# Kernel optimization log

Hardware: AMD Instinct MI355X
Metric: run time of the kernel (lower is better)

The kernel has to match this reference:

```python
import jax, jax.numpy as jnp
import numpy as np
from functools import partial

BETA = 0.9
THR = 1.0
NUM_STEPS = 50
SLOPE = 15.0
BN_EPS = 1e-5
NHID = 250
NCLS = 10

@jax.custom_vjp
def spike_fn(x):
    return (x > 0).astype(x.dtype)

def _spike_fwd(x):
    return spike_fn(x), x

def _spike_bwd(x, g):
    # snntorch fast_sigmoid surrogate: grad = 1 / (slope*|x| + 1)^2
    return (g / (SLOPE * jnp.abs(x) + 1.0) ** 2,)

spike_fn.defvjp(_spike_fwd, _spike_bwd)

def conv1d(x, w, b, stride=1):
    # x: [B,C,L], w: [O,I,K]
    y = jax.lax.conv_general_dilated(x, w, (stride,), 'VALID',
                                     dimension_numbers=('NCH', 'OIH', 'NCH'))
    return y + b[None, :, None]

def bn_eval(x, g, b, m, v):
    inv = g / jnp.sqrt(v + BN_EPS)
    return (x - m[None, :, None]) * inv[None, :, None] + b[None, :, None]

def lif_step(mem, cur):
    # snntorch Leaky (reset_mechanism='subtract'): reset uses detached spike of previous mem
    reset = jax.lax.stop_gradient((mem > THR).astype(mem.dtype))
    mem = BETA * mem + cur - reset * THR
    spk = spike_fn(mem - THR)
    return mem, spk

def maxpool4(x):
    # MaxPool1d(4) on [B,C,L]
    return jax.lax.reduce_window(x, -jnp.inf, jax.lax.max, (1, 1, 4), (1, 1, 4), 'VALID')

def get_embedding(x, c1w, c1b, bn1g, bn1b, bn1m, bn1v, c2w, c2b, bn2g, bn2b, bn2m, bn2v,
                  fc1w, fc1b, fcsw, fcsb):
    B = x.shape[0]
    # input-invariant part of the per-step loop (conv1+BN1 on x)
    cur1 = bn_eval(conv1d(x, c1w, c1b, stride=4), bn1g, bn1b, bn1m, bn1v)  # [B,16,1981]

    def step(carry, _):
        mem1, mem2, mem3 = carry
        mem1, spk1 = lif_step(mem1, cur1)
        pooled = maxpool4(spk1)                                   # [B,16,495]
        cur2 = bn_eval(conv1d(pooled, c2w, c2b), bn2g, bn2b, bn2m, bn2v)  # [B,32,493]
        mem2, spk2 = lif_step(mem2, cur2)
        flat = spk2.reshape(B, -1)                                # [B,15776]
        cur3 = flat @ fc1w.T + fc1b                               # dropout is eval -> identity
        mem3, spk3 = lif_step(mem3, cur3)
        return (mem1, mem2, mem3), spk3

    carry0 = (jnp.zeros_like(cur1),
              jnp.zeros((B, 32, 493), cur1.dtype),
              jnp.zeros((B, NHID), cur1.dtype))
    _, spk_rec = jax.lax.scan(step, carry0, None, length=NUM_STEPS)  # [T,B,250]

    firing_rate = spk_rec.sum(axis=0)                                 # [B,250]
    latency = jnp.argmax(spk_rec, axis=0).astype(x.dtype) / NUM_STEPS # first-spike idx
    comb = jnp.concatenate([firing_rate, latency], axis=1)            # [B,500]
    out = comb @ fcsw.T + fcsb                                        # [B,128]
    norm = jnp.maximum(jnp.linalg.norm(out, axis=1, keepdims=True), 1e-12)
    return out / norm

def setup_inputs() -> dict:
    key = jax.random.key(0)
    ks = jax.random.split(key, 16)
    B, L = 32, 8000
    d = {}
    d['x1'] = jax.random.normal(ks[0], (B, 1, L), jnp.float32)
    d['x2'] = jax.random.normal(ks[1], (B, 1, L), jnp.float32)
    d['c1w'] = jax.random.normal(ks[2], (16, 1, 80), jnp.float32) * 0.1
    d['c1b'] = jax.random.normal(ks[3], (16,), jnp.float32) * 0.1
    d['bn1g'] = jnp.ones((16,), jnp.float32)
    d['bn1b'] = jnp.zeros((16,), jnp.float32)
    d['bn1m'] = jax.random.normal(ks[4], (16,), jnp.float32) * 0.1
    d['bn1v'] = jax.random.uniform(ks[5], (16,), jnp.float32, 0.5, 1.5)
    d['c2w'] = jax.random.normal(ks[6], (32, 16, 3), jnp.float32) * 0.1
    d['c2b'] = jax.random.normal(ks[7], (32,), jnp.float32) * 0.1
    d['bn2g'] = jnp.ones((32,), jnp.float32)
    d['bn2b'] = jnp.zeros((32,), jnp.float32)
    d['bn2m'] = jax.random.normal(ks[8], (32,), jnp.float32) * 0.1
    d['bn2v'] = jax.random.uniform(ks[9], (32,), jnp.float32, 0.5, 1.5)
    d['fc1w'] = jax.random.normal(ks[10], (NHID, 15776), jnp.float32) * 0.02
    d['fc1b'] = jax.random.normal(ks[11], (NHID,), jnp.float32) * 0.02
    d['fcsw'] = jax.random.normal(ks[12], (128, 2 * NHID), jnp.float32) * 0.05
    d['fcsb'] = jax.random.normal(ks[13], (128,), jnp.float32) * 0.05
    return d

def reference(x1, x2, c1w, c1b, bn1g, bn1b, bn1m, bn1v, c2w, c2b, bn2g, bn2b, bn2m, bn2v,
              fc1w, fc1b, fcsw, fcsb):
    params = (c1w, c1b, bn1g, bn1b, bn1m, bn1v, c2w, c2b, bn2g, bn2b, bn2m, bn2v,
              fc1w, fc1b, fcsw, fcsb)
    emb1 = get_embedding(x1, *params)
    emb2 = get_embedding(x2, *params)
    return (emb1, emb2)
```

## Files before the change

kernel.cpp:

```cpp
#include <hip/hip_runtime.h>
#include <math.h>
#include <stdint.h>

#define BETA 0.9f
#define THR 1.0f
#define T_STEPS 50
#define BN_EPS 1e-5f

#define NITEM 64
#define C1 16
#define L1 1981
#define L1P 1984
#define P4 495
#define C2 32
#define L2 493
#define L2PAD 496
#define KTOT 15872
#define KREAL 15776
#define NFC 250
#define NPAD 256
#define KSPLIT 16
#define KRANGE 992
#define KSTEPS 31
#define NKTILE 496
#define MROWS 3200
#define TSLICE 1015808

#define OFF_CUR1 0UL
#define OFF_POOL 8126464UL
#define OFF_SPK2 34340864UL
#define OFF_WT   85131264UL
#define OFF_PART 101384192UL
#define OFF_COMB 127598592UL
#define OFF_CUR3 16384UL

typedef __attribute__((ext_vector_type(8))) short bf16x8;
typedef __attribute__((ext_vector_type(4))) float f32x4;

__device__ __forceinline__ uint32_t f32_to_bf16_rne(float f) {
  uint32_t u = __float_as_uint(f);
  return (u + 0x7FFFu + ((u >> 16) & 1u)) >> 16;
}

__device__ __forceinline__ bf16x8 frag_from_bytes(uint2 a) {
  union { uint32_t u[4]; bf16x8 v; } c;
  c.u[0] = (a.x & 0x00010001u) * 0x3F80u;
  c.u[1] = ((a.x >> 8) & 0x00010001u) * 0x3F80u;
  c.u[2] = (a.y & 0x00010001u) * 0x3F80u;
  c.u[3] = ((a.y >> 8) & 0x00010001u) * 0x3F80u;
  return c.v;
}

__global__ __launch_bounds__(256) void k_wt(const float* __restrict__ fc1w,
                                            uint8_t* __restrict__ wTf) {
  int kt = blockIdx.x;
  int n = threadIdx.x;
  int wv = n >> 6, ni = (n >> 4) & 3, r16 = n & 15;
  uint32_t h16[32], l16[32];
#pragma unroll
  for (int kl = 0; kl < 32; ++kl) {
    int k = kt * 32 + kl;
    int oc = k / L2PAD;
    int pos = k - oc * L2PAD;
    float w = 0.f;
    if (pos < L2 && n < NFC) w = fc1w[n * KREAL + oc * L2 + pos];
    uint32_t hb = f32_to_bf16_rne(w);
    float hf = __uint_as_float(hb << 16);
    h16[kl] = hb;
    l16[kl] = f32_to_bf16_rne(w - hf);
  }
  uint8_t* tb = wTf + (size_t)kt * 32768 + wv * 8192 + ni * 2048;
#pragma unroll
  for (int g = 0; g < 4; ++g) {
    int b = g * 8;
    uint4 h;
    h.x = h16[b + 0] | (h16[b + 2] << 16);
    h.y = h16[b + 1] | (h16[b + 3] << 16);
    h.z = h16[b + 4] | (h16[b + 6] << 16);
    h.w = h16[b + 5] | (h16[b + 7] << 16);
    *reinterpret_cast<uint4*>(tb + (g * 16 + r16) * 16) = h;
    uint4 l;
    l.x = l16[b + 0] | (l16[b + 2] << 16);
    l.y = l16[b + 1] | (l16[b + 3] << 16);
    l.z = l16[b + 4] | (l16[b + 6] << 16);
    l.w = l16[b + 5] | (l16[b + 7] << 16);
    *reinterpret_cast<uint4*>(tb + 1024 + (g * 16 + r16) * 16) = l;
  }
}

__global__ __launch_bounds__(256) void k_conv1(const float* __restrict__ x1, const float* __restrict__ x2,
                                               const float* __restrict__ c1w, const float* __restrict__ c1b,
                                               const float* __restrict__ g, const float* __restrict__ bb,
                                               const float* __restrict__ mn, const float* __restrict__ vr,
                                               float* __restrict__ cur1) {
  __shared__ __align__(16) float xs[1104];
  int item = blockIdx.y;
  int pc = blockIdx.x;
  int tid = threadIdx.x;
  const float* x = (item < 32 ? x1 : x2) + (item & 31) * 8000;
  int xoff = pc * 1024;
  for (int i = tid; i < 1100; i += 256) {
    int gi = xoff + i;
    xs[i] = (gi < 8000) ? x[gi] : 0.f;
  }
  __syncthreads();
  int p = pc * 256 + tid;
  bool pv = (p < L1);
  const float4* xs4 = reinterpret_cast<const float4*>(xs);
  for (int c = 0; c < C1; ++c) {
    float s = g[c] / sqrtf(vr[c] + BN_EPS);
    float sh = (c1b[c] - mn[c]) * s + bb[c];
    const float4* w4 = reinterpret_cast<const float4*>(c1w + c * 80);
    float acc = 0.f;
#pragma unroll
    for (int k4 = 0; k4 < 20; ++k4) {
      float4 wv4 = w4[k4];
      float4 xv = xs4[tid + k4];
      acc += wv4.x * xv.x; acc += wv4.y * xv.y;
      acc += wv4.z * xv.z; acc += wv4.w * xv.w;
    }
    if (pv) cur1[(item * C1 + c) * L1P + p] = acc * s + sh;
  }
}

__global__ __launch_bounds__(256) void k_lif1(const float* __restrict__ cur1,
                                              uint8_t* __restrict__ pooledT) {
  int item = blockIdx.y;
  int g = threadIdx.x & 3;
  int p4 = blockIdx.x * 64 + (threadIdx.x >> 2);
  if (p4 >= P4) return;
  float4 cv[4];
#pragma unroll
  for (int j = 0; j < 4; ++j)
    cv[j] = *reinterpret_cast<const float4*>(cur1 + ((size_t)item * C1 + g * 4 + j) * L1P + 4 * p4);
  float m[4][4];
#pragma unroll
  for (int j = 0; j < 4; ++j)
#pragma unroll
    for (int r = 0; r < 4; ++r) m[j][r] = 0.f;
  uint32_t* out = reinterpret_cast<uint32_t*>(pooledT + ((size_t)item * 50 * 512 + p4) * 16 + g * 4);
  for (int t = 0; t < T_STEPS; ++t) {
    uint32_t pk = 0;
#pragma unroll
    for (int j = 0; j < 4; ++j) {
      int s = 0;
#pragma unroll
      for (int r = 0; r < 4; ++r) {
        float rst = (m[j][r] > THR) ? 1.f : 0.f;
        float cvv = (r == 0) ? cv[j].x : (r == 1) ? cv[j].y : (r == 2) ? cv[j].z : cv[j].w;
        m[j][r] = BETA * m[j][r] + cvv - rst;
        s |= (m[j][r] > THR);
      }
      pk |= ((uint32_t)s) << (8 * j);
    }
    out[t * 2048] = pk;
  }
}

__global__ __launch_bounds__(256) void k_conv2(const uint8_t* __restrict__ pooledT,
                                               const float* __restrict__ c2w, const float* __restrict__ c2b,
                                               const float* __restrict__ g, const float* __restrict__ bb,
                                               const float* __restrict__ mn, const float* __restrict__ vr,
                                               uint32_t* __restrict__ spk2) {
  int item = blockIdx.y;
  int pt = blockIdx.x;
  int tid = threadIdx.x;
  int lane = tid & 63, wv = tid >> 6;
  int r16 = lane & 15, kg = lane >> 4;
  bf16x8 bw[2][2][2];
  float sh[2];
#pragma unroll
  for (int nt = 0; nt < 2; ++nt) {
    int oc = nt * 16 + r16;
    float s2 = g[oc] * rsqrtf(vr[oc] + BN_EPS);
    sh[nt] = (c2b[oc] - mn[oc]) * s2 + bb[oc];
#pragma unroll
    for (int kt = 0; kt < 2; ++kt) {
      uint32_t h[8], l[8];
#pragma unroll
      for (int j = 0; j < 8; ++j) {
        int k = kt * 32 + kg * 8 + j;
        int tap = k >> 4, ic = k & 15;
        float raw = (tap < 3) ? c2w[oc * 48 + ic * 3 + tap] * s2 : 0.f;
        uint32_t hb = f32_to_bf16_rne(raw);
        float hf = __uint_as_float(hb << 16);
        h[j] = hb;
        l[j] = f32_to_bf16_rne(raw - hf);
      }
      union { uint32_t u[4]; bf16x8 v; } ch_, cl_;
      ch_.u[0] = h[0] | (h[2] << 16); ch_.u[1] = h[1] | (h[3] << 16);
      ch_.u[2] = h[4] | (h[6] << 16); ch_.u[3] = h[5] | (h[7] << 16);
      cl_.u[0] = l[0] | (l[2] << 16); cl_.u[1] = l[1] | (l[3] << 16);
      cl_.u[2] = l[4] | (l[6] << 16); cl_.u[3] = l[5] | (l[7] << 16);
      bw[nt][kt][0] = ch_.v;
      bw[nt][kt][1] = cl_.v;
    }
  }
  const uint8_t* base = pooledT + (size_t)item * 50 * 8192;
  int rowA = pt * 64 + wv * 16 + r16;
  size_t off0 = (size_t)(rowA + (kg >> 1)) * 16 + 8 * (kg & 1);
  size_t off1 = (size_t)(rowA + 2) * 16 + 8 * (kg & 1);
  uint2 na0 = *reinterpret_cast<const uint2*>(base + off0);
  uint2 na1 = *reinterpret_cast<const uint2*>(base + off1);
  float mem[2][4] = {{0.f, 0.f, 0.f, 0.f}, {0.f, 0.f, 0.f, 0.f}};
  int pos_base = pt * 64 + wv * 16 + kg * 4;
  bool dostore = pos_base < L2PAD;
  int k0a = r16 * L2PAD + pos_base;
  int k0b = (16 + r16) * L2PAD + pos_base;
  uint32_t sidx0 = (uint32_t)(k0a >> 5) * 512u + (uint32_t)item * 8u + ((uint32_t)(k0a >> 2) & 7u);
  uint32_t sidx1 = (uint32_t)(k0b >> 5) * 512u + (uint32_t)item * 8u + ((uint32_t)(k0b >> 2) & 7u);
  for (int t = 0; t < T_STEPS; ++t) {
    uint2 a0 = na0, a1 = na1;
    const uint8_t* nb = base + (size_t)((t + 1 < T_STEPS) ? t + 1 : t) * 8192;
    na0 = *reinterpret_cast<const uint2*>(nb + off0);
    na1 = *reinterpret_cast<const uint2*>(nb + off1);
    bf16x8 af0 = frag_from_bytes(a0);
    bf16x8 af1 = frag_from_bytes(a1);
    uint32_t st[2];
#pragma unroll
    for (int nt = 0; nt < 2; ++nt) {
      f32x4 acc = (f32x4){0.f, 0.f, 0.f, 0.f};
      acc = __builtin_amdgcn_mfma_f32_16x16x32_bf16(af0, bw[nt][0][0], acc, 0, 0, 0);
      acc = __builtin_amdgcn_mfma_f32_16x16x32_bf16(af1, bw[nt][1][0], acc, 0, 0, 0);
      acc = __builtin_amdgcn_mfma_f32_16x16x32_bf16(af0, bw[nt][0][1], acc, 0, 0, 0);
      acc = __builtin_amdgcn_mfma_f32_16x16x32_bf16(af1, bw[nt][1][1], acc, 0, 0, 0);
      uint32_t packed = 0;
#pragma unroll
      for (int r = 0; r < 4; ++r) {
        float rst = (mem[nt][r] > THR) ? 1.f : 0.f;
        mem[nt][r] = BETA * mem[nt][r] + (acc[r] + sh[nt]) - rst;
        packed |= (mem[nt][r] > THR ? 1u : 0u) << (8 * r);
      }
      st[nt] = packed;
    }
    if (dostore) {
      uint32_t tb = (uint32_t)t * (TSLICE / 4);
      spk2[tb + sidx0] = st[0];
      spk2[tb + sidx1] = st[1];
    }
  }
}

__global__ __launch_bounds__(512) void k_fc1(const uint8_t* __restrict__ spk2,
                                             const uint8_t* __restrict__ wTf,
                                             float* __restrict__ part0,
                                             float* __restrict__ part1) {
  int ks = blockIdx.x;
  int mt = blockIdx.y;
  int tid = threadIdx.x;
  int lane = tid & 63, w8 = tid >> 6;
  int wv = w8 & 3, mg = w8 >> 2;
  int r16 = lane & 15, kg = lane >> 4;
  int t = mt * 2 + mg;

  f32x4 acc[4][4];
#pragma unroll
  for (int mi = 0; mi < 4; ++mi)
#pragma unroll
    for (int ni = 0; ni < 4; ++ni) acc[mi][ni] = (f32x4){0.f, 0.f, 0.f, 0.f};

  const uint8_t* abase = spk2 + (size_t)t * TSLICE + (size_t)(ks * KSTEPS) * 2048 + r16 * 32 + kg * 8;
  const uint8_t* bbase = wTf + (size_t)ks * KSTEPS * 32768 + wv * 8192 + lane * 16;

  for (int ch = 0; ch < KSTEPS; ++ch) {
    uint2 a[4];
#pragma unroll
    for (int mi = 0; mi < 4; ++mi)
      a[mi] = *reinterpret_cast<const uint2*>(abase + (size_t)ch * 2048 + mi * 512);
    bf16x8 bfr[4][2];
#pragma unroll
    for (int ni = 0; ni < 4; ++ni)
#pragma unroll
      for (int sel = 0; sel < 2; ++sel)
        bfr[ni][sel] = *reinterpret_cast<const bf16x8*>(bbase + (size_t)ch * 32768 + ni * 2048 + sel * 1024);
    bf16x8 af[4];
#pragma unroll
    for (int mi = 0; mi < 4; ++mi) af[mi] = frag_from_bytes(a[mi]);
#pragma unroll
    for (int ni = 0; ni < 4; ++ni)
#pragma unroll
      for (int mi = 0; mi < 4; ++mi) {
        acc[mi][ni] = __builtin_amdgcn_mfma_f32_16x16x32_bf16(af[mi], bfr[ni][0], acc[mi][ni], 0, 0, 0);
        acc[mi][ni] = __builtin_amdgcn_mfma_f32_16x16x32_bf16(af[mi], bfr[ni][1], acc[mi][ni], 0, 0, 0);
      }
  }
  float* pb = (ks < 8) ? (part0 + (size_t)ks * MROWS * NPAD)
                       : (part1 + (size_t)(ks - 8) * MROWS * NPAD);
  int colb = wv * 64 + r16;
  int rowb = t * 64 + kg * 4;
#pragma unroll
  for (int mi = 0; mi < 4; ++mi)
#pragma unroll
    for (int ni = 0; ni < 4; ++ni) {
      float* pp = pb + (size_t)(rowb + mi * 16) * NPAD + colb + ni * 16;
#pragma unroll
      for (int r = 0; r < 4; ++r) pp[r * NPAD] = acc[mi][ni][r];
    }
}

__global__ __launch_bounds__(256) void k_red(const float* __restrict__ part0,
                                             const float* __restrict__ part1,
                                             float* __restrict__ cur3) {
  int i = blockIdx.x * 256 + threadIdx.x;
  float s = 0.f;
#pragma unroll
  for (int ksx = 0; ksx < 8; ++ksx) s += part0[(size_t)ksx * MROWS * NPAD + i];
#pragma unroll
  for (int ksx = 0; ksx < 8; ++ksx) s += part1[(size_t)ksx * MROWS * NPAD + i];
  cur3[i] = s;
}

__global__ __launch_bounds__(256) void k_lif3(const float* __restrict__ cur3,
                                              const float* __restrict__ fc1b,
                                              float* __restrict__ comb) {
  int item = blockIdx.x;
  int n = threadIdx.x;
  if (n >= NFC) return;
  float bias = fc1b[n];
  float sv[T_STEPS];
#pragma unroll
  for (int t = 0; t < T_STEPS; ++t)
    sv[t] = cur3[(size_t)(t * NITEM + item) * NPAD + n];
  float mem = 0.f, cnt = 0.f;
  int first = -1;
#pragma unroll
  for (int t = 0; t < T_STEPS; ++t) {
    float r = (mem > THR) ? 1.f : 0.f;
    mem = BETA * mem + (bias + sv[t]) - r;
    if (mem > THR) { cnt += 1.f; if (first < 0) first = t; }
  }
  comb[item * 500 + n] = cnt;
  comb[item * 500 + NFC + n] = (first < 0) ? 0.f : ((float)first / (float)T_STEPS);
}

__global__ __launch_bounds__(128) void k_head(const float* __restrict__ comb,
                                              const float* __restrict__ fcsw,
                                              const float* __restrict__ fcsb,
                                              float* __restrict__ dout) {
  __shared__ float cr[500];
  __shared__ float red[2];
  int item = blockIdx.x;
  int o = threadIdx.x;
  for (int i = o; i < 500; i += 128) cr[i] = comb[item * 500 + i];
  __syncthreads();
  float acc = fcsb[o];
  for (int j = 0; j < 500; ++j) acc += cr[j] * fcsw[o * 500 + j];
  float sq = acc * acc;
  for (int off = 32; off > 0; off >>= 1) sq += __shfl_down(sq, off, 64);
  if ((o & 63) == 0) red[o >> 6] = sq;
  __syncthreads();
  float norm = sqrtf(red[0] + red[1]);
  norm = fmaxf(norm, 1e-12f);
  dout[item * 128 + o] = acc / norm;
}

extern "C" void kernel_launch(void* const* d_in, const int* in_sizes, int n_in,
                              void* d_out, int out_size, void* d_ws, size_t ws_size,
                              hipStream_t stream) {
  const float* x1   = (const float*)d_in[0];
  const float* x2   = (const float*)d_in[1];
  const float* c1w  = (const float*)d_in[2];
  const float* c1b  = (const float*)d_in[3];
  const float* bn1g = (const float*)d_in[4];
  const float* bn1b = (const float*)d_in[5];
  const float* bn1m = (const float*)d_in[6];
  const float* bn1v = (const float*)d_in[7];
  const float* c2w  = (const float*)d_in[8];
  const float* c2b  = (const float*)d_in[9];
  const float* bn2g = (const float*)d_in[10];
  const float* bn2b = (const float*)d_in[11];
  const float* bn2m = (const float*)d_in[12];
  const float* bn2v = (const float*)d_in[13];
  const float* fc1w = (const float*)d_in[14];
  const float* fc1b = (const float*)d_in[15];
  const float* fcsw = (const float*)d_in[16];
  const float* fcsb = (const float*)d_in[17];

  char* ws = (char*)d_ws;
  float*    cur1    = (float*)(ws + OFF_CUR1);
  float*    cur3    = (float*)(ws + OFF_CUR1 + OFF_CUR3);
  uint8_t*  pooledT = (uint8_t*)(ws + OFF_POOL);
  float*    part1   = (float*)(ws + OFF_POOL);
  uint8_t*  spk2    = (uint8_t*)(ws + OFF_SPK2);
  uint8_t*  wTf     = (uint8_t*)(ws + OFF_WT);
  float*    part0   = (float*)(ws + OFF_PART);
  float*    comb    = (float*)(ws + OFF_COMB);

  k_wt<<<dim3(NKTILE), dim3(256), 0, stream>>>(fc1w, wTf);
  k_conv1<<<dim3(8, NITEM), dim3(256), 0, stream>>>(x1, x2, c1w, c1b, bn1g, bn1b, bn1m, bn1v, cur1);
  k_lif1<<<dim3(8, NITEM), dim3(256), 0, stream>>>(cur1, pooledT);
  k_conv2<<<dim3(8, NITEM), dim3(256), 0, stream>>>(pooledT, c2w, c2b, bn2g, bn2b, bn2m, bn2v,
                                                    (uint32_t*)spk2);
  k_fc1<<<dim3(KSPLIT, T_STEPS / 2), dim3(512), 0, stream>>>(spk2, wTf, part0, part1);
  k_red<<<dim3(MROWS * NPAD / 256), dim3(256), 0, stream>>>(part0, part1, cur3);
  k_lif3<<<dim3(NITEM), dim3(256), 0, stream>>>(cur3, fc1b, comb);
  k_head<<<dim3(NITEM), dim3(128), 0, stream>>>(comb, fcsw, fcsb, (float*)d_out);
}
```

Before: 198.7 us.

## Split conv2 output channels and fc1 N-tiles across more waves

k_conv2 now runs 512 threads per block, with each wave computing a single 16-channel output tile instead of both, which doubles wave-level parallelism and halves per-thread registers. k_fc1 gives each block a single time step and splits N across wave pairs, so each wave holds a 4x2 accumulator tile and the grid grows to 16x50 blocks. The aim is more occupancy and latency hiding in both kernels. The cost is redundant A-fragment loads, since both waves of a pair now read the same spike data, and fewer MFMAs per load in fc1.

```diff
diff --git a/kernel.cpp b/kernel.cpp
--- a/kernel.cpp
+++ b/kernel.cpp
@@ -157,7 +157,7 @@
   }
 }
 
-__global__ __launch_bounds__(256) void k_conv2(const uint8_t* __restrict__ pooledT,
+__global__ __launch_bounds__(512) void k_conv2(const uint8_t* __restrict__ pooledT,
                                                const float* __restrict__ c2w, const float* __restrict__ c2b,
                                                const float* __restrict__ g, const float* __restrict__ bb,
                                                const float* __restrict__ mn, const float* __restrict__ vr,
@@ -165,15 +165,16 @@
   int item = blockIdx.y;
   int pt = blockIdx.x;
   int tid = threadIdx.x;
-  int lane = tid & 63, wv = tid >> 6;
+  int lane = tid & 63, w8 = tid >> 6;
+  int wp = w8 >> 1;
+  int nt = w8 & 1;
   int r16 = lane & 15, kg = lane >> 4;
-  bf16x8 bw[2][2][2];
-  float sh[2];
-#pragma unroll
-  for (int nt = 0; nt < 2; ++nt) {
+  bf16x8 bw[2][2];
+  float sh;
+  {
     int oc = nt * 16 + r16;
     float s2 = g[oc] * rsqrtf(vr[oc] + BN_EPS);
-    sh[nt] = (c2b[oc] - mn[oc]) * s2 + bb[oc];
+    sh = (c2b[oc] - mn[oc]) * s2 + bb[oc];
 #pragma unroll
     for (int kt = 0; kt < 2; ++kt) {
       uint32_t h[8], l[8];
@@ -192,23 +193,21 @@
       ch_.u[2] = h[4] | (h[6] << 16); ch_.u[3] = h[5] | (h[7] << 16);
       cl_.u[0] = l[0] | (l[2] << 16); cl_.u[1] = l[1] | (l[3] << 16);
       cl_.u[2] = l[4] | (l[6] << 16); cl_.u[3] = l[5] | (l[7] << 16);
-      bw[nt][kt][0] = ch_.v;
-      bw[nt][kt][1] = cl_.v;
+      bw[kt][0] = ch_.v;
+      bw[kt][1] = cl_.v;
     }
   }
   const uint8_t* base = pooledT + (size_t)item * 50 * 8192;
-  int rowA = pt * 64 + wv * 16 + r16;
+  int rowA = pt * 64 + wp * 16 + r16;
   size_t off0 = (size_t)(rowA + (kg >> 1)) * 16 + 8 * (kg & 1);
   size_t off1 = (size_t)(rowA + 2) * 16 + 8 * (kg & 1);
   uint2 na0 = *reinterpret_cast<const uint2*>(base + off0);
   uint2 na1 = *reinterpret_cast<const uint2*>(base + off1);
-  float mem[2][4] = {{0.f, 0.f, 0.f, 0.f}, {0.f, 0.f, 0.f, 0.f}};
-  int pos_base = pt * 64 + wv * 16 + kg * 4;
+  float mem[4] = {0.f, 0.f, 0.f, 0.f};
+  int pos_base = pt * 64 + wp * 16 + kg * 4;
   bool dostore = pos_base < L2PAD;
-  int k0a = r16 * L2PAD + pos_base;
-  int k0b = (16 + r16) * L2PAD + pos_base;
-  uint32_t sidx0 = (uint32_t)(k0a >> 5) * 512u + (uint32_t)item * 8u + ((uint32_t)(k0a >> 2) & 7u);
-  uint32_t sidx1 = (uint32_t)(k0b >> 5) * 512u + (uint32_t)item * 8u + ((uint32_t)(k0b >> 2) & 7u);
+  int k0 = (nt * 16 + r16) * L2PAD + pos_base;
+  uint32_t sidx = (uint32_t)(k0 >> 5) * 512u + (uint32_t)item * 8u + ((uint32_t)(k0 >> 2) & 7u);
   for (int t = 0; t < T_STEPS; ++t) {
     uint2 a0 = na0, a1 = na1;
     const uint8_t* nb = base + (size_t)((t + 1 < T_STEPS) ? t + 1 : t) * 8192;
@@ -216,28 +215,19 @@
     na1 = *reinterpret_cast<const uint2*>(nb + off1);
     bf16x8 af0 = frag_from_bytes(a0);
     bf16x8 af1 = frag_from_bytes(a1);
-    uint32_t st[2];
-#pragma unroll
-    for (int nt = 0; nt < 2; ++nt) {
-      f32x4 acc = (f32x4){0.f, 0.f, 0.f, 0.f};
-      acc = __builtin_amdgcn_mfma_f32_16x16x32_bf16(af0, bw[nt][0][0], acc, 0, 0, 0);
-      acc = __builtin_amdgcn_mfma_f32_16x16x32_bf16(af1, bw[nt][1][0], acc, 0, 0, 0);
-      acc = __builtin_amdgcn_mfma_f32_16x16x32_bf16(af0, bw[nt][0][1], acc, 0, 0, 0);
-      acc = __builtin_amdgcn_mfma_f32_16x16x32_bf16(af1, bw[nt][1][1], acc, 0, 0, 0);
-      uint32_t packed = 0;
-#pragma unroll
-      for (int r = 0; r < 4; ++r) {
-        float rst = (mem[nt][r] > THR) ? 1.f : 0.f;
-        mem[nt][r] = BETA * mem[nt][r] + (acc[r] + sh[nt]) - rst;
-        packed |= (mem[nt][r] > THR ? 1u : 0u) << (8 * r);
-      }
-      st[nt] = packed;
-    }
-    if (dostore) {
-      uint32_t tb = (uint32_t)t * (TSLICE / 4);
-      spk2[tb + sidx0] = st[0];
-      spk2[tb + sidx1] = st[1];
-    }
+    f32x4 acc = (f32x4){0.f, 0.f, 0.f, 0.f};
+    acc = __builtin_amdgcn_mfma_f32_16x16x32_bf16(af0, bw[0][0], acc, 0, 0, 0);
+    acc = __builtin_amdgcn_mfma_f32_16x16x32_bf16(af1, bw[1][0], acc, 0, 0, 0);
+    acc = __builtin_amdgcn_mfma_f32_16x16x32_bf16(af0, bw[0][1], acc, 0, 0, 0);
+    acc = __builtin_amdgcn_mfma_f32_16x16x32_bf16(af1, bw[1][1], acc, 0, 0, 0);
+    uint32_t packed = 0;
+#pragma unroll
+    for (int r = 0; r < 4; ++r) {
+      float rst = (mem[r] > THR) ? 1.f : 0.f;
+      mem[r] = BETA * mem[r] + (acc[r] + sh) - rst;
+      packed |= (mem[r] > THR ? 1u : 0u) << (8 * r);
+    }
+    if (dostore) spk2[(uint32_t)t * (TSLICE / 4) + sidx] = packed;
   }
 }
 
@@ -246,30 +236,29 @@
                                              float* __restrict__ part0,
                                              float* __restrict__ part1) {
   int ks = blockIdx.x;
-  int mt = blockIdx.y;
+  int t  = blockIdx.y;
   int tid = threadIdx.x;
   int lane = tid & 63, w8 = tid >> 6;
-  int wv = w8 & 3, mg = w8 >> 2;
+  int wv = w8 >> 1, nh = w8 & 1;
   int r16 = lane & 15, kg = lane >> 4;
-  int t = mt * 2 + mg;
-
-  f32x4 acc[4][4];
+
+  f32x4 acc[4][2];
 #pragma unroll
   for (int mi = 0; mi < 4; ++mi)
 #pragma unroll
-    for (int ni = 0; ni < 4; ++ni) acc[mi][ni] = (f32x4){0.f, 0.f, 0.f, 0.f};
+    for (int ni = 0; ni < 2; ++ni) acc[mi][ni] = (f32x4){0.f, 0.f, 0.f, 0.f};
 
   const uint8_t* abase = spk2 + (size_t)t * TSLICE + (size_t)(ks * KSTEPS) * 2048 + r16 * 32 + kg * 8;
-  const uint8_t* bbase = wTf + (size_t)ks * KSTEPS * 32768 + wv * 8192 + lane * 16;
+  const uint8_t* bbase = wTf + (size_t)ks * KSTEPS * 32768 + wv * 8192 + nh * 4096 + lane * 16;
 
   for (int ch = 0; ch < KSTEPS; ++ch) {
     uint2 a[4];
 #pragma unroll
     for (int mi = 0; mi < 4; ++mi)
       a[mi] = *reinterpret_cast<const uint2*>(abase + (size_t)ch * 2048 + mi * 512);
-    bf16x8 bfr[4][2];
-#pragma unroll
-    for (int ni = 0; ni < 4; ++ni)
+    bf16x8 bfr[2][2];
+#pragma unroll
+    for (int ni = 0; ni < 2; ++ni)
 #pragma unroll
       for (int sel = 0; sel < 2; ++sel)
         bfr[ni][sel] = *reinterpret_cast<const bf16x8*>(bbase + (size_t)ch * 32768 + ni * 2048 + sel * 1024);
@@ -277,7 +266,7 @@
 #pragma unroll
     for (int mi = 0; mi < 4; ++mi) af[mi] = frag_from_bytes(a[mi]);
 #pragma unroll
-    for (int ni = 0; ni < 4; ++ni)
+    for (int ni = 0; ni < 2; ++ni)
 #pragma unroll
       for (int mi = 0; mi < 4; ++mi) {
         acc[mi][ni] = __builtin_amdgcn_mfma_f32_16x16x32_bf16(af[mi], bfr[ni][0], acc[mi][ni], 0, 0, 0);
@@ -286,12 +275,12 @@
   }
   float* pb = (ks < 8) ? (part0 + (size_t)ks * MROWS * NPAD)
                        : (part1 + (size_t)(ks - 8) * MROWS * NPAD);
-  int colb = wv * 64 + r16;
+  int colb = wv * 64 + nh * 32 + r16;
   int rowb = t * 64 + kg * 4;
 #pragma unroll
   for (int mi = 0; mi < 4; ++mi)
 #pragma unroll
-    for (int ni = 0; ni < 4; ++ni) {
+    for (int ni = 0; ni < 2; ++ni) {
       float* pp = pb + (size_t)(rowb + mi * 16) * NPAD + colb + ni * 16;
 #pragma unroll
       for (int r = 0; r < 4; ++r) pp[r * NPAD] = acc[mi][ni][r];
@@ -389,9 +378,9 @@
   k_wt<<<dim3(NKTILE), dim3(256), 0, stream>>>(fc1w, wTf);
   k_conv1<<<dim3(8, NITEM), dim3(256), 0, stream>>>(x1, x2, c1w, c1b, bn1g, bn1b, bn1m, bn1v, cur1);
   k_lif1<<<dim3(8, NITEM), dim3(256), 0, stream>>>(cur1, pooledT);
-  k_conv2<<<dim3(8, NITEM), dim3(256), 0, stream>>>(pooledT, c2w, c2b, bn2g, bn2b, bn2m, bn2v,
+  k_conv2<<<dim3(8, NITEM), dim3(512), 0, stream>>>(pooledT, c2w, c2b, bn2g, bn2b, bn2m, bn2v,
                                                     (uint32_t*)spk2);
-  k_fc1<<<dim3(KSPLIT, T_STEPS / 2), dim3(512), 0, stream>>>(spk2, wTf, part0, part1);
+  k_fc1<<<dim3(KSPLIT, T_STEPS), dim3(512), 0, stream>>>(spk2, wTf, part0, part1);
   k_red<<<dim3(MROWS * NPAD / 256), dim3(256), 0, stream>>>(part0, part1, cur3);
   k_lif3<<<dim3(NITEM), dim3(256), 0, stream>>>(cur3, fc1b, comb);
   k_head<<<dim3(NITEM), dim3(128), 0, stream>>>(comb, fcsw, fcsb, (float*)d_out);
```

Measured after the change: 213.9 us. +7.6%, slower.
